# Kernel tuning notes

Measured on AMD Instinct MI355X. Metric: run time of the kernel, lower is better.

The kernel has to match this reference:

```python
import jax, jax.numpy as jnp
import numpy as np

N = 60000   # nodes
E = 200000  # edges
D = 128     # hidden_dim
H = 4       # heads
C = 128     # out_channels per head (concat=False)
L = 3       # num_layers
VA = 128    # atom vocab
VB = 16     # bond vocab
NEG_SLOPE = 0.2


def setup_inputs():
    key = jax.random.key(0)
    ks = jax.random.split(key, 12)
    f = lambda k, s: (jax.random.normal(k, s, jnp.float32) * 0.05)
    return dict(
        x=jax.random.randint(ks[0], (N,), 0, VA),
        edge_index=jax.random.randint(ks[1], (2, E), 0, N),
        edge_attr=jax.random.randint(ks[2], (E,), 0, VB),
        atom_emb=f(ks[3], (VA, D)),
        bond_emb=f(ks[4], (VB, D)),
        Wl=f(ks[5], (L, D, H * C)), bl=jnp.zeros((L, H * C), jnp.float32),
        Wr=f(ks[6], (L, D, H * C)), br=jnp.zeros((L, H * C), jnp.float32),
        We=f(ks[7], (L, D, H * C)),
        att=f(ks[8], (L, H, C)),
        bias=jnp.zeros((L, C), jnp.float32),
        Wa=f(ks[9], (D, VA)), ba=jnp.zeros((VA,), jnp.float32),
        Wb=f(ks[10], (2 * D, VB)), bb=jnp.zeros((VB,), jnp.float32),
    )


def _gatv2_layer(h, e, src, dst, Wl, bl, Wr, br, We, att, bias):
    # GATv2Conv (PyG), eval mode (dropout off), concat=False -> mean over heads
    xl = (h @ Wl + bl).reshape(N, H, C)   # source transform (lin_l)
    xr = (h @ Wr + br).reshape(N, H, C)   # target transform (lin_r)
    ee = (e @ We).reshape(E, H, C)        # edge projection (lin_edge, no bias)
    m = jax.nn.leaky_relu(xl[src] + xr[dst] + ee, NEG_SLOPE)  # [E,H,C]
    logits = jnp.einsum('ehc,hc->eh', m, att)                 # [E,H]
    # segment-softmax over incoming edges of each target node
    mx = jax.ops.segment_max(logits, dst, num_segments=N)
    a = jnp.exp(logits - mx[dst])
    s = jax.ops.segment_sum(a, dst, num_segments=N)
    alpha = a / (s[dst] + 1e-16)
    agg = jax.ops.segment_sum(alpha[:, :, None] * xl[src], dst, num_segments=N)
    return agg.mean(axis=1) + bias  # [N,D]


def reference(x, edge_index, edge_attr, atom_emb, bond_emb,
              Wl, bl, Wr, br, We, att, bias, Wa, ba, Wb, bb):
    src, dst = edge_index[0], edge_index[1]
    h = atom_emb[x]          # [N,D]
    e = bond_emb[edge_attr]  # [E,D]
    for l in range(L):
        upd = _gatv2_layer(h, e, src, dst, Wl[l], bl[l], Wr[l], br[l],
                           We[l], att[l], bias[l])
        h = h + jax.nn.relu(upd)
    atom_logits = h @ Wa + ba                              # [N,VA]
    pair = jnp.concatenate([h[src], h[dst]], axis=-1)      # [E,2D]
    bond_logits = pair @ Wb + bb                           # [E,VB]
    return atom_logits, bond_logits
```

## Files before the change

### kernel.cpp

```cpp
#include <hip/hip_runtime.h>
#include <hip/hip_bf16.h>
#include <math.h>

#define NN 60000
#define NE 200000
#define DD 128
#define NH 4
#define HC 512
#define NL 3
#define VAv 128
#define VBv 16
#define SCAN_CHUNK 512

typedef __attribute__((ext_vector_type(8))) short bf16x8;
typedef __attribute__((ext_vector_type(4))) float f32x4;

__device__ __forceinline__ float bf2f(unsigned short u){
    union{unsigned int i; float f;} v; v.i = ((unsigned int)u)<<16; return v.f;
}
__device__ __forceinline__ unsigned short f2bf(float f){
    union{float f; unsigned int i;} v; v.f = f;
    unsigned int r = v.i + 0x7fffu + ((v.i>>16)&1u);
    return (unsigned short)(r>>16);
}

#define GLOAD_LDS16(g, l) \
    __builtin_amdgcn_global_load_lds((const __attribute__((address_space(1))) void*)(g), \
                                     (__attribute__((address_space(3))) void*)(l), 16, 0, 0)

__global__ void k_embed(const int* __restrict__ x, const float* __restrict__ atom_emb,
                        float* __restrict__ h, unsigned short* __restrict__ hb) {
    int idx = blockIdx.x*blockDim.x + threadIdx.x;
    if (idx >= NN*(DD/4)) return;
    int n = idx >> 5;
    int c4 = idx & 31;
    int a = x[n];
    float4 v = ((const float4*)(atom_emb + (size_t)a*DD))[c4];
    ((float4*)(h + (size_t)n*DD))[c4] = v;
    ushort4 u = make_ushort4(f2bf(v.x), f2bf(v.y), f2bf(v.z), f2bf(v.w));
    ((ushort4*)(hb + (size_t)n*DD))[c4] = u;
}

__global__ void k_convw(const float* __restrict__ Wl, const float* __restrict__ Wr,
                        const float* __restrict__ bl, const float* __restrict__ br,
                        unsigned short* __restrict__ Wlrt, float* __restrict__ blr) {
    int t = blockIdx.x*256 + threadIdx.x;
    if (t < NL*1024*DD) {
        int l = t / (1024*DD);
        int r = t % (1024*DD);
        int n = r / DD;
        int k = r % DD;
        float v = (n < HC) ? Wl[(size_t)l*DD*HC + (size_t)k*HC + n]
                           : Wr[(size_t)l*DD*HC + (size_t)k*HC + (n - HC)];
        Wlrt[t] = f2bf(v);
    }
    if (t < NL*1024) {
        int l = t / 1024, j = t % 1024;
        blr[t] = (j < HC) ? bl[(size_t)l*HC + j] : br[(size_t)l*HC + (j - HC)];
    }
}

__global__ void k_convwa(const float* __restrict__ Wa, unsigned short* __restrict__ Wat) {
    int t = blockIdx.x*256 + threadIdx.x;
    if (t >= DD*VAv) return;
    int n = t / DD;
    int k = t % DD;
    Wat[t] = f2bf(Wa[(size_t)k*VAv + n]);
}

__global__ void k_eproj(const float* __restrict__ bond_emb, const float* __restrict__ We,
                        float* __restrict__ eprojf) {
    int t = blockIdx.x*256 + threadIdx.x;
    if (t >= NL*VBv*HC) return;
    int n = t & (HC-1);
    int v = (t >> 9) & (VBv-1);
    int l = t >> 13;
    const float* be = bond_emb + (size_t)v*DD;
    const float* w  = We + (size_t)l*DD*HC + n;
    float acc = 0.f;
    #pragma unroll 8
    for (int k = 0; k < DD; ++k) acc = fmaf(be[k], w[(size_t)k*HC], acc);
    eprojf[t] = acc;
}

__global__ void k_deg(const int* __restrict__ dst, int* __restrict__ deg) {
    int e = blockIdx.x*blockDim.x + threadIdx.x;
    if (e < NE) atomicAdd(&deg[dst[e]], 1);
}

__global__ void k_scan1(const int* __restrict__ deg, int* __restrict__ exc, int* __restrict__ sums) {
    __shared__ int buf[2][SCAN_CHUNK];
    int t = threadIdx.x;
    int gi = blockIdx.x*SCAN_CHUNK + t;
    int v = (gi < NN) ? deg[gi] : 0;
    buf[0][t] = v;
    __syncthreads();
    int cur = 0;
    for (int off = 1; off < SCAN_CHUNK; off <<= 1) {
        int nv = buf[cur][t] + ((t >= off) ? buf[cur][t-off] : 0);
        buf[cur^1][t] = nv;
        __syncthreads();
        cur ^= 1;
    }
    if (gi < NN) exc[gi] = buf[cur][t] - v;
    if (t == SCAN_CHUNK-1) sums[blockIdx.x] = buf[cur][t];
}

__global__ void k_scan2(int* sums, int nb) {
    __shared__ int buf[2][128];
    int t = threadIdx.x;
    int v = (t < nb) ? sums[t] : 0;
    buf[0][t] = v;
    __syncthreads();
    int cur = 0;
    for (int off = 1; off < 128; off <<= 1) {
        int nv = buf[cur][t] + ((t >= off) ? buf[cur][t-off] : 0);
        buf[cur^1][t] = nv;
        __syncthreads();
        cur ^= 1;
    }
    if (t < nb) sums[t] = buf[cur][t] - v;
}

__global__ void k_scan3(const int* __restrict__ exc, const int* __restrict__ sums,
                        int* __restrict__ rowptr) {
    int i = blockIdx.x*blockDim.x + threadIdx.x;
    if (i < NN) rowptr[i] = exc[i] + sums[i / SCAN_CHUNK];
    if (i == NN) rowptr[NN] = NE;
}

__global__ void k_scatter(const int* __restrict__ srcv, const int* __restrict__ dst,
                          const int* __restrict__ eattr, const int* __restrict__ rowptr,
                          int* __restrict__ cnt, int* __restrict__ packed) {
    int e = blockIdx.x*blockDim.x + threadIdx.x;
    if (e < NE) {
        int d = dst[e];
        int pos = atomicAdd(&cnt[d], 1);
        packed[rowptr[d] + pos] = srcv[e] | (eattr[e] << 16);
    }
}

template<bool OUT_BF16, int MT>
__global__ __launch_bounds__(256)
void k_gemm_mfma(const unsigned short* __restrict__ A,
                 const unsigned short* __restrict__ Bt,
                 const float* __restrict__ bias, void* __restrict__ Cout,
                 int M, int Nc) {
    __shared__ unsigned short As[2][128*128];
    const int tid = threadIdx.x;
    const int lane = tid & 63;
    const int wave = tid >> 6;
    const int bn = blockIdx.x * 128;
    const int bm0 = blockIdx.y * (128*MT);
    const int l15 = lane & 15;
    const int l4  = lane >> 4;
    const int wm = (wave >> 1) * 64;
    const int wn = (wave & 1) * 64;

    bf16x8 bfr[4][4];
    #pragma unroll
    for (int ks = 0; ks < 4; ++ks)
        #pragma unroll
        for (int ni = 0; ni < 4; ++ni)
            bfr[ks][ni] = *(const bf16x8*)(Bt + (size_t)(bn + wn + ni*16 + l15)*128
                                              + (size_t)(ks*4 + l4)*8);

    float4 bv[4];
    #pragma unroll
    for (int ni = 0; ni < 4; ++ni)
        bv[ni] = bias ? *(const float4*)(bias + bn + wn + ni*16 + l4*4)
                      : make_float4(0.f, 0.f, 0.f, 0.f);

    auto stage = [&](int buf, int bm) {
        #pragma unroll
        for (int it = 0; it < 8; ++it) {
            int slot = it*256 + tid;
            int row  = slot >> 4;
            int cph  = slot & 15;
            int clog = cph ^ (row & 15);
            int arow = bm + row; if (arow >= M) arow = M - 1;
            unsigned short* ldst = &As[buf][(size_t)(it*256 + (tid & ~63))*8];
            GLOAD_LDS16(A + (size_t)arow*128 + clog*8, ldst);
        }
    };

    stage(0, bm0);
    asm volatile("s_waitcnt vmcnt(0)" ::: "memory");
    __syncthreads();

    int cur = 0;
    for (int t = 0; t < MT; ++t) {
        int bm = bm0 + t*128;
        if (bm >= M) break;
        bool pf = (t+1 < MT) && (bm + 128 < M);
        if (pf) stage(cur^1, bm + 128);

        f32x4 acc[4][4];
        #pragma unroll
        for (int i = 0; i < 4; ++i)
            #pragma unroll
            for (int j = 0; j < 4; ++j)
                acc[i][j] = (f32x4){0.f, 0.f, 0.f, 0.f};

        #pragma unroll
        for (int ks = 0; ks < 4; ++ks) {
            bf16x8 af[4];
            int cph = (ks*4 + l4) ^ l15;
            #pragma unroll
            for (int mi = 0; mi < 4; ++mi) {
                int row = wm + mi*16 + l15;
                af[mi] = *(const bf16x8*)(&As[cur][(size_t)row*128 + cph*8]);
            }
            #pragma unroll
            for (int mi = 0; mi < 4; ++mi)
                #pragma unroll
                for (int ni = 0; ni < 4; ++ni)
                    acc[mi][ni] = __builtin_amdgcn_mfma_f32_16x16x32_bf16(bfr[ks][ni], af[mi], acc[mi][ni], 0, 0, 0);
        }

        #pragma unroll
        for (int mi = 0; mi < 4; ++mi) {
            int row = bm + wm + mi*16 + l15;
            bool rok = (row < M);
            #pragma unroll
            for (int ni = 0; ni < 4; ++ni) {
                float v0 = acc[mi][ni][0] + bv[ni].x;
                float v1 = acc[mi][ni][1] + bv[ni].y;
                float v2 = acc[mi][ni][2] + bv[ni].z;
                float v3 = acc[mi][ni][3] + bv[ni].w;
                int colb = bn + wn + ni*16 + l4*4;
                if (rok) {
                    if (OUT_BF16) {
                        unsigned int lo, hi;
                        asm("v_cvt_pk_bf16_f32 %0, %1, %2" : "=v"(lo) : "v"(v0), "v"(v1));
                        asm("v_cvt_pk_bf16_f32 %0, %1, %2" : "=v"(hi) : "v"(v2), "v"(v3));
                        *(uint2*)((unsigned short*)Cout + (size_t)row*Nc + colb) = make_uint2(lo, hi);
                    } else {
                        *(float4*)((float*)Cout + (size_t)row*Nc + colb) = make_float4(v0, v1, v2, v3);
                    }
                }
            }
        }

        if (pf) {
            asm volatile("s_waitcnt vmcnt(16)" ::: "memory");
            __builtin_amdgcn_s_barrier();
        }
        cur ^= 1;
    }
}

__global__ __launch_bounds__(512)
void k_aggregate(const unsigned short* __restrict__ xlr,
                 const float* __restrict__ eprojf,
                 const int* __restrict__ rowptr, const int* __restrict__ packed,
                 const float* __restrict__ att,
                 const float* __restrict__ bias,
                 float* __restrict__ h, unsigned short* __restrict__ hb) {
    __shared__ float eps[VBv*HC];
    {
        const float4* s4 = (const float4*)eprojf;
        float4* d4 = (float4*)eps;
        int t = threadIdx.x;
        #pragma unroll
        for (int i = 0; i < 4; ++i) d4[t + i*512] = s4[t + i*512];
    }
    __syncthreads();

    int wave = threadIdx.x >> 6;
    int lane = threadIdx.x & 63;
    int n = blockIdx.x*8 + wave;
    int loff = lane*8;

    float xrf[8], attf[8];
    {
        bf16x8 xv = *(const bf16x8*)(xlr + (size_t)n*1024 + 512 + loff);
        #pragma unroll
        for (int u = 0; u < 8; ++u) xrf[u] = bf2f((unsigned short)xv[u]);
        float4 a0 = *(const float4*)(att + loff);
        float4 a1 = *(const float4*)(att + loff + 4);
        attf[0]=a0.x; attf[1]=a0.y; attf[2]=a0.z; attf[3]=a0.w;
        attf[4]=a1.x; attf[5]=a1.y; attf[6]=a1.z; attf[7]=a1.w;
    }

    float acc[8] = {0,0,0,0,0,0,0,0};
    float wsum = 0.f;
    int beg = rowptr[n], end = rowptr[n+1];

    int p = beg;
    for (; p + 2 <= end; p += 2) {
        int pk0 = packed[p], pk1 = packed[p+1];
        int s0 = pk0 & 0xFFFF, ea0 = pk0 >> 16;
        int s1 = pk1 & 0xFFFF, ea1 = pk1 >> 16;
        bf16x8 v0 = *(const bf16x8*)(xlr + (size_t)s0*1024 + loff);
        bf16x8 v1 = *(const bf16x8*)(xlr + (size_t)s1*1024 + loff);
        const float* ep0 = eps + ea0*HC + loff;
        const float* ep1 = eps + ea1*HC + loff;
        float4 e00 = *(const float4*)ep0, e01 = *(const float4*)(ep0+4);
        float4 e10 = *(const float4*)ep1, e11 = *(const float4*)(ep1+4);
        float xf0[8], xf1[8], epa[8], epb[8];
        epa[0]=e00.x; epa[1]=e00.y; epa[2]=e00.z; epa[3]=e00.w;
        epa[4]=e01.x; epa[5]=e01.y; epa[6]=e01.z; epa[7]=e01.w;
        epb[0]=e10.x; epb[1]=e10.y; epb[2]=e10.z; epb[3]=e10.w;
        epb[4]=e11.x; epb[5]=e11.y; epb[6]=e11.z; epb[7]=e11.w;
        float p0 = 0.f, p1 = 0.f;
        #pragma unroll
        for (int u = 0; u < 8; ++u) {
            xf0[u] = bf2f((unsigned short)v0[u]);
            xf1[u] = bf2f((unsigned short)v1[u]);
            float z0 = xf0[u] + xrf[u] + epa[u];
            float z1 = xf1[u] + xrf[u] + epb[u];
            p0 = fmaf(fmaxf(z0, 0.2f*z0), attf[u], p0);
            p1 = fmaf(fmaxf(z1, 0.2f*z1), attf[u], p1);
        }
        p0 += __shfl_xor(p0, 1); p1 += __shfl_xor(p1, 1);
        p0 += __shfl_xor(p0, 2); p1 += __shfl_xor(p1, 2);
        p0 += __shfl_xor(p0, 4); p1 += __shfl_xor(p1, 4);
        p0 += __shfl_xor(p0, 8); p1 += __shfl_xor(p1, 8);
        float w0 = __expf(p0), w1 = __expf(p1);
        wsum += w0 + w1;
        #pragma unroll
        for (int u = 0; u < 8; ++u) {
            acc[u] = fmaf(w0, xf0[u], acc[u]);
            acc[u] = fmaf(w1, xf1[u], acc[u]);
        }
    }
    if (p < end) {
        int pk0 = packed[p];
        int s0 = pk0 & 0xFFFF, ea0 = pk0 >> 16;
        bf16x8 v0 = *(const bf16x8*)(xlr + (size_t)s0*1024 + loff);
        const float* ep0 = eps + ea0*HC + loff;
        float4 e00 = *(const float4*)ep0, e01 = *(const float4*)(ep0+4);
        float epa[8];
        epa[0]=e00.x; epa[1]=e00.y; epa[2]=e00.z; epa[3]=e00.w;
        epa[4]=e01.x; epa[5]=e01.y; epa[6]=e01.z; epa[7]=e01.w;
        float xf0[8];
        float p0 = 0.f;
        #pragma unroll
        for (int u = 0; u < 8; ++u) {
            xf0[u] = bf2f((unsigned short)v0[u]);
            float z0 = xf0[u] + xrf[u] + epa[u];
            p0 = fmaf(fmaxf(z0, 0.2f*z0), attf[u], p0);
        }
        p0 += __shfl_xor(p0, 1);
        p0 += __shfl_xor(p0, 2);
        p0 += __shfl_xor(p0, 4);
        p0 += __shfl_xor(p0, 8);
        float w0 = __expf(p0);
        wsum += w0;
        #pragma unroll
        for (int u = 0; u < 8; ++u) acc[u] = fmaf(w0, xf0[u], acc[u]);
    }

    float inv = __builtin_amdgcn_rcpf(wsum + 1e-16f);
    float rr[8];
    #pragma unroll
    for (int u = 0; u < 8; ++u) rr[u] = acc[u] * inv;
    #pragma unroll
    for (int u = 0; u < 8; ++u) rr[u] += __shfl_xor(rr[u], 16);
    #pragma unroll
    for (int u = 0; u < 8; ++u) rr[u] += __shfl_xor(rr[u], 32);

    if (lane < 16) {
        int c = lane*8;
        float* hp = h + (size_t)n*DD + c;
        float4 h0 = *(const float4*)hp;
        float4 h1 = *(const float4*)(hp + 4);
        float4 b0 = *(const float4*)(bias + c);
        float4 b1 = *(const float4*)(bias + c + 4);
        float o[8];
        o[0] = h0.x + fmaxf(0.f, fmaf(0.25f, rr[0], b0.x));
        o[1] = h0.y + fmaxf(0.f, fmaf(0.25f, rr[1], b0.y));
        o[2] = h0.z + fmaxf(0.f, fmaf(0.25f, rr[2], b0.z));
        o[3] = h0.w + fmaxf(0.f, fmaf(0.25f, rr[3], b0.w));
        o[4] = h1.x + fmaxf(0.f, fmaf(0.25f, rr[4], b1.x));
        o[5] = h1.y + fmaxf(0.f, fmaf(0.25f, rr[5], b1.y));
        o[6] = h1.z + fmaxf(0.f, fmaf(0.25f, rr[6], b1.z));
        o[7] = h1.w + fmaxf(0.f, fmaf(0.25f, rr[7], b1.w));
        *(float4*)hp       = make_float4(o[0], o[1], o[2], o[3]);
        *(float4*)(hp + 4) = make_float4(o[4], o[5], o[6], o[7]);
        ushort4 u0 = make_ushort4(f2bf(o[0]), f2bf(o[1]), f2bf(o[2]), f2bf(o[3]));
        ushort4 u1 = make_ushort4(f2bf(o[4]), f2bf(o[5]), f2bf(o[6]), f2bf(o[7]));
        unsigned short* hbp = hb + (size_t)n*DD + c;
        *(ushort4*)hbp       = u0;
        *(ushort4*)(hbp + 4) = u1;
    }
}

__global__ __launch_bounds__(256)
void k_bond(const unsigned short* __restrict__ hb,
            const int* __restrict__ srcv, const int* __restrict__ dstv,
            const float* __restrict__ Wb, const float* __restrict__ bb,
            float* __restrict__ out) {
    int e = blockIdx.x*256 + threadIdx.x;
    if (e >= NE) return;
    int s = srcv[e], d = dstv[e];
    const bf16x8* hs = (const bf16x8*)(hb + (size_t)s*DD);
    const bf16x8* hd = (const bf16x8*)(hb + (size_t)d*DD);
    float acc[16];
    #pragma unroll
    for (int j = 0; j < 16; ++j) acc[j] = bb[j];
    for (int c = 0; c < 16; ++c) {
        bf16x8 v = hs[c];
        #pragma unroll
        for (int u = 0; u < 8; ++u) {
            float a = bf2f((unsigned short)v[u]);
            const float* w = Wb + (size_t)(c*8 + u)*16;
            #pragma unroll
            for (int j = 0; j < 16; ++j) acc[j] = fmaf(a, w[j], acc[j]);
        }
    }
    for (int c = 0; c < 16; ++c) {
        bf16x8 v = hd[c];
        #pragma unroll
        for (int u = 0; u < 8; ++u) {
            float a = bf2f((unsigned short)v[u]);
            const float* w = Wb + (size_t)(128 + c*8 + u)*16;
            #pragma unroll
            for (int j = 0; j < 16; ++j) acc[j] = fmaf(a, w[j], acc[j]);
        }
    }
    float4* o = (float4*)(out + (size_t)e*16);
    o[0] = make_float4(acc[0],  acc[1],  acc[2],  acc[3]);
    o[1] = make_float4(acc[4],  acc[5],  acc[6],  acc[7]);
    o[2] = make_float4(acc[8],  acc[9],  acc[10], acc[11]);
    o[3] = make_float4(acc[12], acc[13], acc[14], acc[15]);
}

extern "C" void kernel_launch(void* const* d_in, const int* in_sizes, int n_in,
                              void* d_out, int out_size, void* d_ws, size_t ws_size,
                              hipStream_t stream) {
    const int*   x        = (const int*)d_in[0];
    const int*   edge_idx = (const int*)d_in[1];
    const int*   eattr    = (const int*)d_in[2];
    const float* atom_emb = (const float*)d_in[3];
    const float* bond_emb = (const float*)d_in[4];
    const float* Wl  = (const float*)d_in[5];
    const float* bl  = (const float*)d_in[6];
    const float* Wr  = (const float*)d_in[7];
    const float* br  = (const float*)d_in[8];
    const float* We  = (const float*)d_in[9];
    const float* att = (const float*)d_in[10];
    const float* bias= (const float*)d_in[11];
    const float* Wa  = (const float*)d_in[12];
    const float* ba  = (const float*)d_in[13];
    const float* Wb  = (const float*)d_in[14];
    const float* bb  = (const float*)d_in[15];

    const int* src = edge_idx;
    const int* dst = edge_idx + NE;

    char* p = (char*)d_ws;
    auto alloc = [&](size_t bytes) -> void* {
        void* r = p; p += (bytes + 255) & ~(size_t)255; return r;
    };
    float*          h      = (float*)alloc((size_t)NN*DD*4);
    unsigned short* hb     = (unsigned short*)alloc((size_t)NN*DD*2);
    unsigned short* xlr    = (unsigned short*)alloc((size_t)NN*1024*2);
    unsigned short* Wlrt   = (unsigned short*)alloc((size_t)NL*1024*DD*2);
    float*          blr    = (float*)alloc((size_t)NL*1024*4);
    unsigned short* Wat    = (unsigned short*)alloc((size_t)DD*VAv*2);
    float*          eprojf = (float*)alloc((size_t)NL*VBv*HC*4);
    int*            deg    = (int*)alloc((size_t)NN*4);
    int*            exc    = (int*)alloc((size_t)NN*4);
    int*            sums   = (int*)alloc(256*4);
    int*            rowptr = (int*)alloc((size_t)(NN+1)*4);
    int*            cnt    = (int*)alloc((size_t)NN*4);
    int*            packed = (int*)alloc((size_t)NE*4);

    float* atom_out = (float*)d_out;
    float* bond_out = atom_out + (size_t)NN*VAv;

    hipMemsetAsync(deg, 0, (size_t)NN*4, stream);
    hipMemsetAsync(cnt, 0, (size_t)NN*4, stream);

    k_embed<<<7500, 256, 0, stream>>>(x, atom_emb, h, hb);
    k_convw<<<(NL*1024*DD + 255)/256, 256, 0, stream>>>(Wl, Wr, bl, br, Wlrt, blr);
    k_convwa<<<(DD*VAv + 255)/256, 256, 0, stream>>>(Wa, Wat);
    k_eproj<<<(NL*VBv*HC + 255)/256, 256, 0, stream>>>(bond_emb, We, eprojf);

    int nchunks = (NN + SCAN_CHUNK - 1) / SCAN_CHUNK;
    k_deg<<<(NE+255)/256, 256, 0, stream>>>(dst, deg);
    k_scan1<<<nchunks, SCAN_CHUNK, 0, stream>>>(deg, exc, sums);
    k_scan2<<<1, 128, 0, stream>>>(sums, nchunks);
    k_scan3<<<(NN+256)/256, 256, 0, stream>>>(exc, sums, rowptr);
    k_scatter<<<(NE+255)/256, 256, 0, stream>>>(src, dst, eattr, rowptr, cnt, packed);

    const int MTILES = (NN + 127) / 128;
    const int GRP4 = (MTILES + 3) / 4;
    const int GRP2 = (MTILES + 1) / 2;
    for (int l = 0; l < NL; ++l) {
        const float* att_l  = att  + (size_t)l*NH*VAv;
        const float* bias_l = bias + (size_t)l*DD;
        const unsigned short* Wlrt_l = Wlrt + (size_t)l*1024*DD;
        const float* blr_l = blr + (size_t)l*1024;
        const float* ep_l  = eprojf + (size_t)l*VBv*HC;

        k_gemm_mfma<true, 4><<<dim3(1024/128, GRP4), 256, 0, stream>>>(hb, Wlrt_l, blr_l, xlr, NN, 1024);
        k_aggregate<<<NN/8, 512, 0, stream>>>(xlr, ep_l, rowptr, packed, att_l, bias_l, h, hb);
    }

    k_gemm_mfma<false, 2><<<dim3(VAv/128, GRP2), 256, 0, stream>>>(hb, Wat, ba, atom_out, NN, VAv);
    k_bond<<<(NE+255)/256, 256, 0, stream>>>(hb, src, dst, Wb, bb, bond_out);
}
```

Measured before the change: 469.7 us.

## Persist aggregate blocks, swizzle edge-projection LDS layout, unroll edges by four

The aggregate kernel now runs as a grid-stride loop over 2500 blocks instead of 7500, so each block's 32KB shared-memory copy of the edge projection table is loaded fewer times. The edge projection table is stored permuted so each lane reads two float4s at lane*4 and 256+lane*4, which avoids LDS bank conflicts from the stride-8 per-lane reads. The inner edge loop is unrolled by four so more gathers are in flight at once. The cost is more register pressure and possible load imbalance across the persistent blocks.

```diff
diff --git a/kernel.cpp b/kernel.cpp
--- a/kernel.cpp
+++ b/kernel.cpp
@@ -69,7 +69,7 @@
 }
 
 __global__ void k_eproj(const float* __restrict__ bond_emb, const float* __restrict__ We,
-                        float* __restrict__ eprojf) {
+                        float* __restrict__ eprojd) {
     int t = blockIdx.x*256 + threadIdx.x;
     if (t >= NL*VBv*HC) return;
     int n = t & (HC-1);
@@ -80,7 +80,9 @@
     float acc = 0.f;
     #pragma unroll 8
     for (int k = 0; k < DD; ++k) acc = fmaf(be[k], w[(size_t)k*HC], acc);
-    eprojf[t] = acc;
+    int ln = n >> 3, u = n & 7;
+    int pos = (u >> 2)*256 + ln*4 + (u & 3);
+    eprojd[((size_t)l*VBv + v)*HC + pos] = acc;
 }
 
 __global__ void k_deg(const int* __restrict__ dst, int* __restrict__ deg) {
@@ -252,14 +254,14 @@
 
 __global__ __launch_bounds__(512)
 void k_aggregate(const unsigned short* __restrict__ xlr,
-                 const float* __restrict__ eprojf,
+                 const float* __restrict__ eprojd,
                  const int* __restrict__ rowptr, const int* __restrict__ packed,
                  const float* __restrict__ att,
                  const float* __restrict__ bias,
                  float* __restrict__ h, unsigned short* __restrict__ hb) {
     __shared__ float eps[VBv*HC];
     {
-        const float4* s4 = (const float4*)eprojf;
+        const float4* s4 = (const float4*)eprojd;
         float4* d4 = (float4*)eps;
         int t = threadIdx.x;
         #pragma unroll
@@ -267,124 +269,129 @@
     }
     __syncthreads();
 
-    int wave = threadIdx.x >> 6;
-    int lane = threadIdx.x & 63;
-    int n = blockIdx.x*8 + wave;
-    int loff = lane*8;
-
-    float xrf[8], attf[8];
+    const int wave = threadIdx.x >> 6;
+    const int lane = threadIdx.x & 63;
+    const int loff = lane*8;
+    const int l4x  = lane*4;
+
+    float attf[8];
     {
-        bf16x8 xv = *(const bf16x8*)(xlr + (size_t)n*1024 + 512 + loff);
-        #pragma unroll
-        for (int u = 0; u < 8; ++u) xrf[u] = bf2f((unsigned short)xv[u]);
         float4 a0 = *(const float4*)(att + loff);
         float4 a1 = *(const float4*)(att + loff + 4);
         attf[0]=a0.x; attf[1]=a0.y; attf[2]=a0.z; attf[3]=a0.w;
         attf[4]=a1.x; attf[5]=a1.y; attf[6]=a1.z; attf[7]=a1.w;
     }
 
-    float acc[8] = {0,0,0,0,0,0,0,0};
-    float wsum = 0.f;
-    int beg = rowptr[n], end = rowptr[n+1];
-
-    int p = beg;
-    for (; p + 2 <= end; p += 2) {
-        int pk0 = packed[p], pk1 = packed[p+1];
-        int s0 = pk0 & 0xFFFF, ea0 = pk0 >> 16;
-        int s1 = pk1 & 0xFFFF, ea1 = pk1 >> 16;
-        bf16x8 v0 = *(const bf16x8*)(xlr + (size_t)s0*1024 + loff);
-        bf16x8 v1 = *(const bf16x8*)(xlr + (size_t)s1*1024 + loff);
-        const float* ep0 = eps + ea0*HC + loff;
-        const float* ep1 = eps + ea1*HC + loff;
-        float4 e00 = *(const float4*)ep0, e01 = *(const float4*)(ep0+4);
-        float4 e10 = *(const float4*)ep1, e11 = *(const float4*)(ep1+4);
-        float xf0[8], xf1[8], epa[8], epb[8];
-        epa[0]=e00.x; epa[1]=e00.y; epa[2]=e00.z; epa[3]=e00.w;
-        epa[4]=e01.x; epa[5]=e01.y; epa[6]=e01.z; epa[7]=e01.w;
-        epb[0]=e10.x; epb[1]=e10.y; epb[2]=e10.z; epb[3]=e10.w;
-        epb[4]=e11.x; epb[5]=e11.y; epb[6]=e11.z; epb[7]=e11.w;
-        float p0 = 0.f, p1 = 0.f;
-        #pragma unroll
-        for (int u = 0; u < 8; ++u) {
-            xf0[u] = bf2f((unsigned short)v0[u]);
-            xf1[u] = bf2f((unsigned short)v1[u]);
-            float z0 = xf0[u] + xrf[u] + epa[u];
-            float z1 = xf1[u] + xrf[u] + epb[u];
-            p0 = fmaf(fmaxf(z0, 0.2f*z0), attf[u], p0);
-            p1 = fmaf(fmaxf(z1, 0.2f*z1), attf[u], p1);
-        }
-        p0 += __shfl_xor(p0, 1); p1 += __shfl_xor(p1, 1);
-        p0 += __shfl_xor(p0, 2); p1 += __shfl_xor(p1, 2);
-        p0 += __shfl_xor(p0, 4); p1 += __shfl_xor(p1, 4);
-        p0 += __shfl_xor(p0, 8); p1 += __shfl_xor(p1, 8);
-        float w0 = __expf(p0), w1 = __expf(p1);
-        wsum += w0 + w1;
-        #pragma unroll
-        for (int u = 0; u < 8; ++u) {
-            acc[u] = fmaf(w0, xf0[u], acc[u]);
-            acc[u] = fmaf(w1, xf1[u], acc[u]);
-        }
-    }
-    if (p < end) {
-        int pk0 = packed[p];
-        int s0 = pk0 & 0xFFFF, ea0 = pk0 >> 16;
-        bf16x8 v0 = *(const bf16x8*)(xlr + (size_t)s0*1024 + loff);
-        const float* ep0 = eps + ea0*HC + loff;
-        float4 e00 = *(const float4*)ep0, e01 = *(const float4*)(ep0+4);
-        float epa[8];
-        epa[0]=e00.x; epa[1]=e00.y; epa[2]=e00.z; epa[3]=e00.w;
-        epa[4]=e01.x; epa[5]=e01.y; epa[6]=e01.z; epa[7]=e01.w;
-        float xf0[8];
-        float p0 = 0.f;
-        #pragma unroll
-        for (int u = 0; u < 8; ++u) {
-            xf0[u] = bf2f((unsigned short)v0[u]);
-            float z0 = xf0[u] + xrf[u] + epa[u];
-            p0 = fmaf(fmaxf(z0, 0.2f*z0), attf[u], p0);
-        }
-        p0 += __shfl_xor(p0, 1);
-        p0 += __shfl_xor(p0, 2);
-        p0 += __shfl_xor(p0, 4);
-        p0 += __shfl_xor(p0, 8);
-        float w0 = __expf(p0);
-        wsum += w0;
-        #pragma unroll
-        for (int u = 0; u < 8; ++u) acc[u] = fmaf(w0, xf0[u], acc[u]);
-    }
-
-    float inv = __builtin_amdgcn_rcpf(wsum + 1e-16f);
-    float rr[8];
-    #pragma unroll
-    for (int u = 0; u < 8; ++u) rr[u] = acc[u] * inv;
-    #pragma unroll
-    for (int u = 0; u < 8; ++u) rr[u] += __shfl_xor(rr[u], 16);
-    #pragma unroll
-    for (int u = 0; u < 8; ++u) rr[u] += __shfl_xor(rr[u], 32);
-
-    if (lane < 16) {
-        int c = lane*8;
-        float* hp = h + (size_t)n*DD + c;
-        float4 h0 = *(const float4*)hp;
-        float4 h1 = *(const float4*)(hp + 4);
-        float4 b0 = *(const float4*)(bias + c);
-        float4 b1 = *(const float4*)(bias + c + 4);
-        float o[8];
-        o[0] = h0.x + fmaxf(0.f, fmaf(0.25f, rr[0], b0.x));
-        o[1] = h0.y + fmaxf(0.f, fmaf(0.25f, rr[1], b0.y));
-        o[2] = h0.z + fmaxf(0.f, fmaf(0.25f, rr[2], b0.z));
-        o[3] = h0.w + fmaxf(0.f, fmaf(0.25f, rr[3], b0.w));
-        o[4] = h1.x + fmaxf(0.f, fmaf(0.25f, rr[4], b1.x));
-        o[5] = h1.y + fmaxf(0.f, fmaf(0.25f, rr[5], b1.y));
-        o[6] = h1.z + fmaxf(0.f, fmaf(0.25f, rr[6], b1.z));
-        o[7] = h1.w + fmaxf(0.f, fmaf(0.25f, rr[7], b1.w));
-        *(float4*)hp       = make_float4(o[0], o[1], o[2], o[3]);
-        *(float4*)(hp + 4) = make_float4(o[4], o[5], o[6], o[7]);
-        ushort4 u0 = make_ushort4(f2bf(o[0]), f2bf(o[1]), f2bf(o[2]), f2bf(o[3]));
-        ushort4 u1 = make_ushort4(f2bf(o[4]), f2bf(o[5]), f2bf(o[6]), f2bf(o[7]));
-        unsigned short* hbp = hb + (size_t)n*DD + c;
-        *(ushort4*)hbp       = u0;
-        *(ushort4*)(hbp + 4) = u1;
-    }
+#define EDGE_PROC(vv, eA, eB) do {                                          \
+        float xf_[8];                                                       \
+        float epv_[8] = {eA.x,eA.y,eA.z,eA.w,eB.x,eB.y,eB.z,eB.w};          \
+        float pz_ = 0.f;                                                    \
+        _Pragma("unroll")                                                   \
+        for (int u = 0; u < 8; ++u) {                                       \
+            xf_[u] = bf2f((unsigned short)vv[u]);                           \
+            float z_ = xf_[u] + xrf[u] + epv_[u];                           \
+            pz_ = fmaf(fmaxf(z_, 0.2f*z_), attf[u], pz_);                   \
+        }                                                                   \
+        pz_ += __shfl_xor(pz_, 1);                                          \
+        pz_ += __shfl_xor(pz_, 2);                                          \
+        pz_ += __shfl_xor(pz_, 4);                                          \
+        pz_ += __shfl_xor(pz_, 8);                                          \
+        float w_ = __expf(pz_);                                             \
+        wsum += w_;                                                         \
+        _Pragma("unroll")                                                   \
+        for (int u = 0; u < 8; ++u) acc[u] = fmaf(w_, xf_[u], acc[u]);      \
+    } while (0)
+
+    for (int g = blockIdx.x; g < NN/8; g += gridDim.x) {
+        int n = g*8 + wave;
+
+        float xrf[8];
+        {
+            bf16x8 xv = *(const bf16x8*)(xlr + (size_t)n*1024 + 512 + loff);
+            #pragma unroll
+            for (int u = 0; u < 8; ++u) xrf[u] = bf2f((unsigned short)xv[u]);
+        }
+
+        float acc[8] = {0,0,0,0,0,0,0,0};
+        float wsum = 0.f;
+        int beg = rowptr[n], end = rowptr[n+1];
+        int p = beg;
+
+        for (; p + 4 <= end; p += 4) {
+            int pk0 = packed[p],   pk1 = packed[p+1];
+            int pk2 = packed[p+2], pk3 = packed[p+3];
+            bf16x8 v0 = *(const bf16x8*)(xlr + (size_t)(pk0 & 0xFFFF)*1024 + loff);
+            bf16x8 v1 = *(const bf16x8*)(xlr + (size_t)(pk1 & 0xFFFF)*1024 + loff);
+            bf16x8 v2 = *(const bf16x8*)(xlr + (size_t)(pk2 & 0xFFFF)*1024 + loff);
+            bf16x8 v3 = *(const bf16x8*)(xlr + (size_t)(pk3 & 0xFFFF)*1024 + loff);
+            const float* e0 = eps + (pk0 >> 16)*HC;
+            const float* e1 = eps + (pk1 >> 16)*HC;
+            const float* e2 = eps + (pk2 >> 16)*HC;
+            const float* e3 = eps + (pk3 >> 16)*HC;
+            float4 eA0 = *(const float4*)(e0 + l4x), eB0 = *(const float4*)(e0 + 256 + l4x);
+            float4 eA1 = *(const float4*)(e1 + l4x), eB1 = *(const float4*)(e1 + 256 + l4x);
+            float4 eA2 = *(const float4*)(e2 + l4x), eB2 = *(const float4*)(e2 + 256 + l4x);
+            float4 eA3 = *(const float4*)(e3 + l4x), eB3 = *(const float4*)(e3 + 256 + l4x);
+            EDGE_PROC(v0, eA0, eB0);
+            EDGE_PROC(v1, eA1, eB1);
+            EDGE_PROC(v2, eA2, eB2);
+            EDGE_PROC(v3, eA3, eB3);
+        }
+        if (p + 2 <= end) {
+            int pk0 = packed[p], pk1 = packed[p+1];
+            bf16x8 v0 = *(const bf16x8*)(xlr + (size_t)(pk0 & 0xFFFF)*1024 + loff);
+            bf16x8 v1 = *(const bf16x8*)(xlr + (size_t)(pk1 & 0xFFFF)*1024 + loff);
+            const float* e0 = eps + (pk0 >> 16)*HC;
+            const float* e1 = eps + (pk1 >> 16)*HC;
+            float4 eA0 = *(const float4*)(e0 + l4x), eB0 = *(const float4*)(e0 + 256 + l4x);
+            float4 eA1 = *(const float4*)(e1 + l4x), eB1 = *(const float4*)(e1 + 256 + l4x);
+            EDGE_PROC(v0, eA0, eB0);
+            EDGE_PROC(v1, eA1, eB1);
+            p += 2;
+        }
+        if (p < end) {
+            int pk0 = packed[p];
+            bf16x8 v0 = *(const bf16x8*)(xlr + (size_t)(pk0 & 0xFFFF)*1024 + loff);
+            const float* e0 = eps + (pk0 >> 16)*HC;
+            float4 eA0 = *(const float4*)(e0 + l4x), eB0 = *(const float4*)(e0 + 256 + l4x);
+            EDGE_PROC(v0, eA0, eB0);
+        }
+
+        float inv = __builtin_amdgcn_rcpf(wsum + 1e-16f);
+        float rr[8];
+        #pragma unroll
+        for (int u = 0; u < 8; ++u) rr[u] = acc[u] * inv;
+        #pragma unroll
+        for (int u = 0; u < 8; ++u) rr[u] += __shfl_xor(rr[u], 16);
+        #pragma unroll
+        for (int u = 0; u < 8; ++u) rr[u] += __shfl_xor(rr[u], 32);
+
+        if (lane < 16) {
+            int c = lane*8;
+            float* hp = h + (size_t)n*DD + c;
+            float4 h0 = *(const float4*)hp;
+            float4 h1 = *(const float4*)(hp + 4);
+            float4 b0 = *(const float4*)(bias + c);
+            float4 b1 = *(const float4*)(bias + c + 4);
+            float o[8];
+            o[0] = h0.x + fmaxf(0.f, fmaf(0.25f, rr[0], b0.x));
+            o[1] = h0.y + fmaxf(0.f, fmaf(0.25f, rr[1], b0.y));
+            o[2] = h0.z + fmaxf(0.f, fmaf(0.25f, rr[2], b0.z));
+            o[3] = h0.w + fmaxf(0.f, fmaf(0.25f, rr[3], b0.w));
+            o[4] = h1.x + fmaxf(0.f, fmaf(0.25f, rr[4], b1.x));
+            o[5] = h1.y + fmaxf(0.f, fmaf(0.25f, rr[5], b1.y));
+            o[6] = h1.z + fmaxf(0.f, fmaf(0.25f, rr[6], b1.z));
+            o[7] = h1.w + fmaxf(0.f, fmaf(0.25f, rr[7], b1.w));
+            *(float4*)hp       = make_float4(o[0], o[1], o[2], o[3]);
+            *(float4*)(hp + 4) = make_float4(o[4], o[5], o[6], o[7]);
+            ushort4 u0 = make_ushort4(f2bf(o[0]), f2bf(o[1]), f2bf(o[2]), f2bf(o[3]));
+            ushort4 u1 = make_ushort4(f2bf(o[4]), f2bf(o[5]), f2bf(o[6]), f2bf(o[7]));
+            unsigned short* hbp = hb + (size_t)n*DD + c;
+            *(ushort4*)hbp       = u0;
+            *(ushort4*)(hbp + 4) = u1;
+        }
+    }
+#undef EDGE_PROC
 }
 
 __global__ __launch_bounds__(256)
@@ -460,7 +467,7 @@
     unsigned short* Wlrt   = (unsigned short*)alloc((size_t)NL*1024*DD*2);
     float*          blr    = (float*)alloc((size_t)NL*1024*4);
     unsigned short* Wat    = (unsigned short*)alloc((size_t)DD*VAv*2);
-    float*          eprojf = (float*)alloc((size_t)NL*VBv*HC*4);
+    float*          eprojd = (float*)alloc((size_t)NL*VBv*HC*4);
     int*            deg    = (int*)alloc((size_t)NN*4);
     int*            exc    = (int*)alloc((size_t)NN*4);
     int*            sums   = (int*)alloc(256*4);
@@ -477,7 +484,7 @@
     k_embed<<<7500, 256, 0, stream>>>(x, atom_emb, h, hb);
     k_convw<<<(NL*1024*DD + 255)/256, 256, 0, stream>>>(Wl, Wr, bl, br, Wlrt, blr);
     k_convwa<<<(DD*VAv + 255)/256, 256, 0, stream>>>(Wa, Wat);
-    k_eproj<<<(NL*VBv*HC + 255)/256, 256, 0, stream>>>(bond_emb, We, eprojf);
+    k_eproj<<<(NL*VBv*HC + 255)/256, 256, 0, stream>>>(bond_emb, We, eprojd);
 
     int nchunks = (NN + SCAN_CHUNK - 1) / SCAN_CHUNK;
     k_deg<<<(NE+255)/256, 256, 0, stream>>>(dst, deg);
@@ -494,10 +501,10 @@
         const float* bias_l = bias + (size_t)l*DD;
         const unsigned short* Wlrt_l = Wlrt + (size_t)l*1024*DD;
         const float* blr_l = blr + (size_t)l*1024;
-        const float* ep_l  = eprojf + (size_t)l*VBv*HC;
+        const float* ep_l  = eprojd + (size_t)l*VBv*HC;
 
         k_gemm_mfma<true, 4><<<dim3(1024/128, GRP4), 256, 0, stream>>>(hb, Wlrt_l, blr_l, xlr, NN, 1024);
-        k_aggregate<<<NN/8, 512, 0, stream>>>(xlr, ep_l, rowptr, packed, att_l, bias_l, h, hb);
+        k_aggregate<<<2500, 512, 0, stream>>>(xlr, ep_l, rowptr, packed, att_l, bias_l, h, hb);
     }
 
     k_gemm_mfma<false, 2><<<dim3(VAv/128, GRP2), 256, 0, stream>>>(hb, Wat, ba, atom_out, NN, VAv);
```

Measured after the change: 472.7 us. No clear change (+0.6%).
